# Performance work log

Hardware: AMD Instinct MI355X
Metric: run time of the kernel (lower is better)

The kernel has to match this reference:

```python
import jax, jax.numpy as jnp
import numpy as np

N = 1024
B = 128
DT = 0.1
STEPS = 10

def setup_inputs() -> dict:
    key = jax.random.key(0)
    k1, k2, k3 = jax.random.split(key, 3)
    theta_init = jax.random.normal(k1, (B, N), dtype=jnp.float32)
    K0 = jax.random.normal(k2, (N, N), dtype=jnp.float32) * 0.1
    K = (K0 + K0.T) / 2  # symmetric coupling matrix, as in __init__
    omega = jax.random.normal(k3, (N,), dtype=jnp.float32) * 0.1
    K_global = jnp.asarray(0.5, dtype=jnp.float32)
    return {"theta_init": theta_init, "K": K, "omega": omega, "K_global": K_global}

def _compute_coherence(theta):
    # Kuramoto order parameter r = |<e^{i theta}>| over oscillator axis
    cos_mean = jnp.cos(theta).mean(axis=-1)
    sin_mean = jnp.sin(theta).mean(axis=-1)
    return jnp.sqrt(cos_mean ** 2 + sin_mean ** 2)

def reference(theta_init, K, omega, K_global):
    n = theta_init.shape[-1]

    def step(theta, _):
        # theta_diff[b, i, j] = theta[b, j] - theta[b, i]
        theta_diff = theta[..., None, :] - theta[..., :, None]  # [B, n, n]
        coupling_sum = (K * jnp.sin(theta_diff)).sum(axis=-1)   # [B, n]
        dtheta = omega + (K_global / n) * coupling_sum
        theta_new = theta + DT * dtheta
        # wrap to (-pi, pi]
        theta_new = jnp.arctan2(jnp.sin(theta_new), jnp.cos(theta_new))
        return theta_new, None

    theta, _ = jax.lax.scan(step, theta_init, None, length=STEPS)
    coherence = _compute_coherence(theta)
    return theta, coherence
```

## Files before the change

### kernel.cpp

```cpp
#include <hip/hip_runtime.h>
#include <math.h>

#define KN 1024
#define KB 128
#define KDT 0.1f
#define KSTEPS 10
#define KMAGIC 0xB0000000u
#define PI_F 3.14159265358979f
#define TWO_PI_F 6.28318530717959f

typedef __attribute__((ext_vector_type(8))) short short8;
typedef __attribute__((ext_vector_type(4))) float floatx4;
typedef unsigned long long u64;

__device__ __forceinline__ unsigned short f2bf(float f) {
    unsigned u = __float_as_uint(f);
    u += 0x7FFF + ((u >> 16) & 1);
    return (unsigned short)(u >> 16);
}

__device__ __forceinline__ unsigned xidx(int grp, int b15, int k) {
    return (unsigned)(grp * 16384 + (k >> 5) * 512 + ((k >> 1) & 3) * 128 +
                      ((k >> 3) & 3) * 32 + b15 * 2 + (k & 1));
}

__global__ __launch_bounds__(512)
void k_main(const float* __restrict__ theta0,
            const float* __restrict__ Kmat,
            const float* __restrict__ omega,
            const float* __restrict__ kg,
            float* __restrict__ out_theta,
            float* __restrict__ out_coh,
            unsigned* __restrict__ flags,
            float* __restrict__ acc,
            unsigned* __restrict__ xA,
            unsigned* __restrict__ xB)
{
    const int grp = blockIdx.x >> 5;
    const int b0  = grp * 16;
    const int i0  = (blockIdx.x & 31) * 32;

    const int tid  = threadIdx.x;
    const int lane = tid & 63;
    const int kq   = tid >> 6;
    const int r16  = lane & 15;
    const int quad = lane >> 4;

    __shared__ float ldsY[8][2][16][34];

    if ((blockIdx.x & 31) == 0 && tid < 16) {
        __hip_atomic_store(&acc[(b0 + tid) * 16], 0.f, __ATOMIC_RELAXED,
                           __HIP_MEMORY_SCOPE_AGENT);
        __hip_atomic_store(&acc[2048 + (b0 + tid) * 16], 0.f, __ATOMIC_RELAXED,
                           __HIP_MEMORY_SCOPE_AGENT);
    }

    short8 bfrag[2][4];
    #pragma unroll
    for (int wi = 0; wi < 2; ++wi) {
        const float* kp = Kmat + (size_t)(i0 + wi * 16 + r16) * KN + kq * 128 + quad * 8;
        #pragma unroll
        for (int it = 0; it < 4; ++it) {
            const float4 v0 = *reinterpret_cast<const float4*>(kp + it * 32);
            const float4 v1 = *reinterpret_cast<const float4*>(kp + it * 32 + 4);
            short8 b_;
            b_[0] = (short)f2bf(v0.x); b_[1] = (short)f2bf(v0.y);
            b_[2] = (short)f2bf(v0.z); b_[3] = (short)f2bf(v0.w);
            b_[4] = (short)f2bf(v1.x); b_[5] = (short)f2bf(v1.y);
            b_[6] = (short)f2bf(v1.z); b_[7] = (short)f2bf(v1.w);
            bfrag[wi][it] = b_;
        }
    }

    const int eb = b0 + (tid >> 5);
    const int ei = i0 + (tid & 31);
    float th_reg = theta0[(size_t)eb * KN + ei];
    const float omg = omega[ei];
    float sn, cs;
    __sincosf(th_reg, &sn, &cs);
    __hip_atomic_store(&xA[xidx(grp, eb & 15, ei)],
                       (unsigned)f2bf(sn) | ((unsigned)f2bf(cs) << 16),
                       __ATOMIC_RELAXED, __HIP_MEMORY_SCOPE_AGENT);
    const float scale = kg[0] * (1.0f / (float)KN);

    __syncthreads();
    if (tid == 0)
        __hip_atomic_store(&flags[blockIdx.x], KMAGIC + 0u,
                           __ATOMIC_RELAXED, __HIP_MEMORY_SCOPE_AGENT);

    auto wait_chunks = [&](unsigned tgt) {
        unsigned polls = 0;
        for (;;) {
            unsigned v = tgt;
            if (lane < 4)
                v = __hip_atomic_load(&flags[grp * 32 + kq * 4 + lane],
                                      __ATOMIC_RELAXED, __HIP_MEMORY_SCOPE_AGENT);
            if (__ballot(v >= tgt) == ~0ull) break;
            if (++polls > 4000000u) break;
            __builtin_amdgcn_s_sleep(2);
        }
    };

    const unsigned* xcur = xA;
    unsigned* xnxt = xB;
    float s2 = sn, c2 = cs;
    for (int s = 0; s < KSTEPS; ++s) {
        wait_chunks(KMAGIC + (unsigned)s);

        const u64* xg = (const u64*)xcur + grp * 8192 + kq * 1024 + lane;
        u64 aw[4][4];
        #pragma unroll
        for (int it = 0; it < 4; ++it)
            #pragma unroll
            for (int jj = 0; jj < 4; ++jj)
                aw[it][jj] = __hip_atomic_load((u64*)(xg + it * 256 + jj * 64),
                                               __ATOMIC_RELAXED,
                                               __HIP_MEMORY_SCOPE_AGENT);
        floatx4 accS[2] = {{0.f,0.f,0.f,0.f},{0.f,0.f,0.f,0.f}};
        floatx4 accC[2] = {{0.f,0.f,0.f,0.f},{0.f,0.f,0.f,0.f}};
        #pragma unroll
        for (int it = 0; it < 4; ++it) {
            short8 a_s, a_c;
            #pragma unroll
            for (int jj = 0; jj < 4; ++jj) {
                unsigned lo = (unsigned)aw[it][jj];
                unsigned hi = (unsigned)(aw[it][jj] >> 32);
                a_s[jj * 2]     = (short)(lo & 0xffffu);
                a_c[jj * 2]     = (short)(lo >> 16);
                a_s[jj * 2 + 1] = (short)(hi & 0xffffu);
                a_c[jj * 2 + 1] = (short)(hi >> 16);
            }
            #pragma unroll
            for (int wi = 0; wi < 2; ++wi) {
                accS[wi] = __builtin_amdgcn_mfma_f32_16x16x32_bf16(a_s, bfrag[wi][it], accS[wi], 0, 0, 0);
                accC[wi] = __builtin_amdgcn_mfma_f32_16x16x32_bf16(a_c, bfrag[wi][it], accC[wi], 0, 0, 0);
            }
        }
        #pragma unroll
        for (int wi = 0; wi < 2; ++wi)
            #pragma unroll
            for (int r = 0; r < 4; ++r) {
                ldsY[kq][0][quad * 4 + r][wi * 16 + r16] = accS[wi][r];
                ldsY[kq][1][quad * 4 + r][wi * 16 + r16] = accC[wi][r];
            }
        __syncthreads();

        {
            const int bl = tid >> 5, ilo = tid & 31;
            float Ys = 0.f, Yc = 0.f;
            #pragma unroll
            for (int q = 0; q < 8; ++q) {
                Ys += ldsY[q][0][bl][ilo];
                Yc += ldsY[q][1][bl][ilo];
            }
            const float coupling = cs * Ys - sn * Yc;
            float tn = th_reg + KDT * (omg + scale * coupling);
            __sincosf(tn, &s2, &c2);
            if (tn > PI_F)       tn -= TWO_PI_F;
            else if (tn < -PI_F) tn += TWO_PI_F;
            th_reg = tn;
            sn = s2; cs = c2;
        }
        if (s < KSTEPS - 1) {
            __hip_atomic_store(&xnxt[xidx(grp, eb & 15, ei)],
                               (unsigned)f2bf(s2) | ((unsigned)f2bf(c2) << 16),
                               __ATOMIC_RELAXED, __HIP_MEMORY_SCOPE_AGENT);
            __syncthreads();
            if (tid == 0)
                __hip_atomic_store(&flags[blockIdx.x], KMAGIC + (unsigned)(s + 1),
                                   __ATOMIC_RELAXED, __HIP_MEMORY_SCOPE_AGENT);
            const unsigned* t = xcur; xcur = xnxt; xnxt = (unsigned*)t;
        } else {
            out_theta[(size_t)eb * KN + ei] = th_reg;
        }
    }

    __syncthreads();
    float* red = &ldsY[0][0][0][0];
    red[tid]       = s2;
    red[512 + tid] = c2;
    __syncthreads();
    if (tid < 16) {
        float ss = 0.f, cc = 0.f;
        #pragma unroll
        for (int il2 = 0; il2 < 32; ++il2) {
            ss += red[tid * 32 + il2];
            cc += red[512 + tid * 32 + il2];
        }
        atomicAdd(&acc[(b0 + tid) * 16], ss);
        atomicAdd(&acc[2048 + (b0 + tid) * 16], cc);
    }
    __syncthreads();
    if (tid == 0)
        __hip_atomic_store(&flags[blockIdx.x], KMAGIC + (unsigned)KSTEPS,
                           __ATOMIC_RELAXED, __HIP_MEMORY_SCOPE_AGENT);

    if ((blockIdx.x & 31) == 0) {
        if (tid < 64) {
            const unsigned tgt = KMAGIC + (unsigned)KSTEPS;
            unsigned polls = 0;
            for (;;) {
                unsigned v = tgt;
                if (lane < 32)
                    v = __hip_atomic_load(&flags[grp * 32 + lane],
                                          __ATOMIC_RELAXED, __HIP_MEMORY_SCOPE_AGENT);
                if (__ballot(v >= tgt) == ~0ull) break;
                if (++polls > 4000000u) break;
                __builtin_amdgcn_s_sleep(2);
            }
        }
        __syncthreads();
        if (tid < 16) {
            float sv = __hip_atomic_load(&acc[(b0 + tid) * 16],
                                         __ATOMIC_RELAXED, __HIP_MEMORY_SCOPE_AGENT);
            float cv = __hip_atomic_load(&acc[2048 + (b0 + tid) * 16],
                                         __ATOMIC_RELAXED, __HIP_MEMORY_SCOPE_AGENT);
            float sm = sv * (1.0f / (float)KN);
            float cm = cv * (1.0f / (float)KN);
            out_coh[b0 + tid] = sqrtf(cm * cm + sm * sm);
        }
    }
}

extern "C" void kernel_launch(void* const* d_in, const int* in_sizes, int n_in,
                              void* d_out, int out_size, void* d_ws, size_t ws_size,
                              hipStream_t stream)
{
    (void)in_sizes; (void)n_in; (void)out_size; (void)ws_size;

    const float* theta0 = (const float*)d_in[0];
    const float* Kmat   = (const float*)d_in[1];
    const float* omega  = (const float*)d_in[2];
    const float* kg     = (const float*)d_in[3];

    float* out_theta = (float*)d_out;
    float* out_coh   = out_theta + (size_t)KB * KN;

    unsigned* flags = (unsigned*)d_ws;
    float* acc      = (float*)((char*)d_ws + 4096);
    unsigned* xA    = (unsigned*)((char*)d_ws + 4096 + 16384);
    unsigned* xB    = xA + (size_t)KB * KN;

    k_main<<<256, 512, 0, stream>>>(theta0, Kmat, omega, kg,
                                    out_theta, out_coh, flags, acc, xA, xB);
}
```

Before: 97.89 us.

## Retile blocks to 8x64, use per-wave flags and multi-buffered exchange

Each block now covers 8 batch rows by 64 oscillators instead of 16 by 32. The packed sin/cos exchange buffer becomes separate bf16 sin and cos planes, so a single MFMA A operand carries sin rows and cos rows together. Readiness is tracked with one flag per wave instead of one per block, which drops the block-wide barrier before publishing, and the exchange buffer is rotated across up to 11 depths when workspace allows, avoiding write-after-read hazards between steps. This aims to cut the inter-block synchronisation latency per step, at the cost of polling more flags and relying on workspace size.

```diff
diff --git a/kernel.cpp b/kernel.cpp
--- a/kernel.cpp
+++ b/kernel.cpp
@@ -17,11 +17,6 @@
     unsigned u = __float_as_uint(f);
     u += 0x7FFF + ((u >> 16) & 1);
     return (unsigned short)(u >> 16);
-}
-
-__device__ __forceinline__ unsigned xidx(int grp, int b15, int k) {
-    return (unsigned)(grp * 16384 + (k >> 5) * 512 + ((k >> 1) & 3) * 128 +
-                      ((k >> 3) & 3) * 32 + b15 * 2 + (k & 1));
 }
 
 __global__ __launch_bounds__(512)
@@ -33,32 +28,34 @@
             float* __restrict__ out_coh,
             unsigned* __restrict__ flags,
             float* __restrict__ acc,
-            unsigned* __restrict__ xA,
-            unsigned* __restrict__ xB)
+            unsigned short* __restrict__ xbuf,
+            int depth)
 {
-    const int grp = blockIdx.x >> 5;
-    const int b0  = grp * 16;
-    const int i0  = (blockIdx.x & 31) * 32;
+    const int grp = blockIdx.x >> 4;
+    const int ib  = blockIdx.x & 15;
+    const int b0  = grp * 8;
+    const int i0  = ib * 64;
 
     const int tid  = threadIdx.x;
     const int lane = tid & 63;
-    const int kq   = tid >> 6;
+    const int wv   = tid >> 6;
     const int r16  = lane & 15;
     const int quad = lane >> 4;
-
-    __shared__ float ldsY[8][2][16][34];
-
-    if ((blockIdx.x & 31) == 0 && tid < 16) {
-        __hip_atomic_store(&acc[(b0 + tid) * 16], 0.f, __ATOMIC_RELAXED,
-                           __HIP_MEMORY_SCOPE_AGENT);
-        __hip_atomic_store(&acc[2048 + (b0 + tid) * 16], 0.f, __ATOMIC_RELAXED,
-                           __HIP_MEMORY_SCOPE_AGENT);
-    }
-
-    short8 bfrag[2][4];
+    const int ub  = lane >> 3;
+    const int ui  = i0 + wv * 8 + (lane & 7);
+    const int uil = wv * 8 + (lane & 7);
+
+    __shared__ float ldsY[8][16][68];
+
+    if (ib == 0 && tid < 8) {
+        __hip_atomic_store(&acc[(b0 + tid) * 16], 0.f, __ATOMIC_RELAXED, __HIP_MEMORY_SCOPE_AGENT);
+        __hip_atomic_store(&acc[2048 + (b0 + tid) * 16], 0.f, __ATOMIC_RELAXED, __HIP_MEMORY_SCOPE_AGENT);
+    }
+
+    short8 bfrag[4][4];
     #pragma unroll
-    for (int wi = 0; wi < 2; ++wi) {
-        const float* kp = Kmat + (size_t)(i0 + wi * 16 + r16) * KN + kq * 128 + quad * 8;
+    for (int sub = 0; sub < 4; ++sub) {
+        const float* kp = Kmat + (size_t)(i0 + sub * 16 + r16) * KN + wv * 128 + quad * 8;
         #pragma unroll
         for (int it = 0; it < 4; ++it) {
             const float4 v0 = *reinterpret_cast<const float4*>(kp + it * 32);
@@ -68,149 +65,129 @@
             b_[2] = (short)f2bf(v0.z); b_[3] = (short)f2bf(v0.w);
             b_[4] = (short)f2bf(v1.x); b_[5] = (short)f2bf(v1.y);
             b_[6] = (short)f2bf(v1.z); b_[7] = (short)f2bf(v1.w);
-            bfrag[wi][it] = b_;
-        }
-    }
-
-    const int eb = b0 + (tid >> 5);
-    const int ei = i0 + (tid & 31);
-    float th_reg = theta0[(size_t)eb * KN + ei];
-    const float omg = omega[ei];
+            bfrag[sub][it] = b_;
+        }
+    }
+
+    float th = theta0[(size_t)(b0 + ub) * KN + ui];
+    const float omg = omega[ui];
+    const float scale = kg[0] * (1.0f / (float)KN);
     float sn, cs;
-    __sincosf(th_reg, &sn, &cs);
-    __hip_atomic_store(&xA[xidx(grp, eb & 15, ei)],
-                       (unsigned)f2bf(sn) | ((unsigned)f2bf(cs) << 16),
-                       __ATOMIC_RELAXED, __HIP_MEMORY_SCOPE_AGENT);
-    const float scale = kg[0] * (1.0f / (float)KN);
-
-    __syncthreads();
-    if (tid == 0)
-        __hip_atomic_store(&flags[blockIdx.x], KMAGIC + 0u,
-                           __ATOMIC_RELAXED, __HIP_MEMORY_SCOPE_AGENT);
-
-    auto wait_chunks = [&](unsigned tgt) {
-        unsigned polls = 0;
-        for (;;) {
-            unsigned v = tgt;
-            if (lane < 4)
-                v = __hip_atomic_load(&flags[grp * 32 + kq * 4 + lane],
-                                      __ATOMIC_RELAXED, __HIP_MEMORY_SCOPE_AGENT);
-            if (__ballot(v >= tgt) == ~0ull) break;
-            if (++polls > 4000000u) break;
-            __builtin_amdgcn_s_sleep(2);
-        }
-    };
-
-    const unsigned* xcur = xA;
-    unsigned* xnxt = xB;
-    float s2 = sn, c2 = cs;
+    __sincosf(th, &sn, &cs);
+
+    const unsigned kblk = (unsigned)(ib * 8 + wv);
+    unsigned* myflag = &flags[grp * 128 + ib * 8 + wv];
+
+    {
+        unsigned short* xp = xbuf + (size_t)grp * 16384 + (size_t)kblk * 128;
+        __hip_atomic_store(&xp[lane],      f2bf(sn), __ATOMIC_RELAXED, __HIP_MEMORY_SCOPE_AGENT);
+        __hip_atomic_store(&xp[64 + lane], f2bf(cs), __ATOMIC_RELAXED, __HIP_MEMORY_SCOPE_AGENT);
+        __builtin_amdgcn_s_waitcnt(0x0F70);
+        if (lane == 0)
+            __hip_atomic_store(myflag, KMAGIC + 0u, __ATOMIC_RELAXED, __HIP_MEMORY_SCOPE_AGENT);
+    }
+
+    floatx4 accv[4];
     for (int s = 0; s < KSTEPS; ++s) {
-        wait_chunks(KMAGIC + (unsigned)s);
-
-        const u64* xg = (const u64*)xcur + grp * 8192 + kq * 1024 + lane;
-        u64 aw[4][4];
-        #pragma unroll
-        for (int it = 0; it < 4; ++it)
+        {
+            const unsigned tgt = KMAGIC + (unsigned)s;
+            unsigned polls = 0;
+            for (;;) {
+                unsigned v = tgt;
+                if (lane < 16)
+                    v = __hip_atomic_load(&flags[grp * 128 + wv * 16 + lane],
+                                          __ATOMIC_RELAXED, __HIP_MEMORY_SCOPE_AGENT);
+                if (__ballot(v >= tgt) == ~0ull) break;
+                if (++polls > 8000000u) break;
+                __builtin_amdgcn_s_sleep(1);
+            }
+        }
+        const u64* xg = (const u64*)(xbuf + (size_t)(s % depth) * 262144) + grp * 4096 + r16 * 2;
+        u64 aw[4][2];
+        #pragma unroll
+        for (int it = 0; it < 4; ++it) {
+            const u64* p = xg + (size_t)(wv * 16 + it * 4 + quad) * 32;
+            aw[it][0] = __hip_atomic_load((u64*)p,       __ATOMIC_RELAXED, __HIP_MEMORY_SCOPE_AGENT);
+            aw[it][1] = __hip_atomic_load((u64*)(p + 1), __ATOMIC_RELAXED, __HIP_MEMORY_SCOPE_AGENT);
+        }
+        #pragma unroll
+        for (int sub = 0; sub < 4; ++sub) accv[sub] = (floatx4){0.f, 0.f, 0.f, 0.f};
+        #pragma unroll
+        for (int it = 0; it < 4; ++it) {
+            union { u64 q[2]; short8 s8; } ua;
+            ua.q[0] = aw[it][0]; ua.q[1] = aw[it][1];
             #pragma unroll
-            for (int jj = 0; jj < 4; ++jj)
-                aw[it][jj] = __hip_atomic_load((u64*)(xg + it * 256 + jj * 64),
-                                               __ATOMIC_RELAXED,
-                                               __HIP_MEMORY_SCOPE_AGENT);
-        floatx4 accS[2] = {{0.f,0.f,0.f,0.f},{0.f,0.f,0.f,0.f}};
-        floatx4 accC[2] = {{0.f,0.f,0.f,0.f},{0.f,0.f,0.f,0.f}};
-        #pragma unroll
-        for (int it = 0; it < 4; ++it) {
-            short8 a_s, a_c;
+            for (int sub = 0; sub < 4; ++sub)
+                accv[sub] = __builtin_amdgcn_mfma_f32_16x16x32_bf16(ua.s8, bfrag[sub][it], accv[sub], 0, 0, 0);
+        }
+        #pragma unroll
+        for (int sub = 0; sub < 4; ++sub)
             #pragma unroll
-            for (int jj = 0; jj < 4; ++jj) {
-                unsigned lo = (unsigned)aw[it][jj];
-                unsigned hi = (unsigned)(aw[it][jj] >> 32);
-                a_s[jj * 2]     = (short)(lo & 0xffffu);
-                a_c[jj * 2]     = (short)(lo >> 16);
-                a_s[jj * 2 + 1] = (short)(hi & 0xffffu);
-                a_c[jj * 2 + 1] = (short)(hi >> 16);
-            }
-            #pragma unroll
-            for (int wi = 0; wi < 2; ++wi) {
-                accS[wi] = __builtin_amdgcn_mfma_f32_16x16x32_bf16(a_s, bfrag[wi][it], accS[wi], 0, 0, 0);
-                accC[wi] = __builtin_amdgcn_mfma_f32_16x16x32_bf16(a_c, bfrag[wi][it], accC[wi], 0, 0, 0);
-            }
-        }
-        #pragma unroll
-        for (int wi = 0; wi < 2; ++wi)
-            #pragma unroll
-            for (int r = 0; r < 4; ++r) {
-                ldsY[kq][0][quad * 4 + r][wi * 16 + r16] = accS[wi][r];
-                ldsY[kq][1][quad * 4 + r][wi * 16 + r16] = accC[wi][r];
-            }
+            for (int r = 0; r < 4; ++r)
+                ldsY[wv][quad * 4 + r][sub * 16 + r16] = accv[sub][r];
         __syncthreads();
 
         {
-            const int bl = tid >> 5, ilo = tid & 31;
             float Ys = 0.f, Yc = 0.f;
             #pragma unroll
             for (int q = 0; q < 8; ++q) {
-                Ys += ldsY[q][0][bl][ilo];
-                Yc += ldsY[q][1][bl][ilo];
+                Ys += ldsY[q][ub][uil];
+                Yc += ldsY[q][8 + ub][uil];
             }
             const float coupling = cs * Ys - sn * Yc;
-            float tn = th_reg + KDT * (omg + scale * coupling);
+            float tn = th + KDT * (omg + scale * coupling);
+            float s2, c2;
             __sincosf(tn, &s2, &c2);
             if (tn > PI_F)       tn -= TWO_PI_F;
             else if (tn < -PI_F) tn += TWO_PI_F;
-            th_reg = tn;
-            sn = s2; cs = c2;
+            th = tn; sn = s2; cs = c2;
         }
         if (s < KSTEPS - 1) {
-            __hip_atomic_store(&xnxt[xidx(grp, eb & 15, ei)],
-                               (unsigned)f2bf(s2) | ((unsigned)f2bf(c2) << 16),
-                               __ATOMIC_RELAXED, __HIP_MEMORY_SCOPE_AGENT);
-            __syncthreads();
-            if (tid == 0)
-                __hip_atomic_store(&flags[blockIdx.x], KMAGIC + (unsigned)(s + 1),
+            unsigned short* xp = xbuf + (size_t)((s + 1) % depth) * 262144
+                               + (size_t)grp * 16384 + (size_t)kblk * 128;
+            __hip_atomic_store(&xp[lane],      f2bf(sn), __ATOMIC_RELAXED, __HIP_MEMORY_SCOPE_AGENT);
+            __hip_atomic_store(&xp[64 + lane], f2bf(cs), __ATOMIC_RELAXED, __HIP_MEMORY_SCOPE_AGENT);
+            __builtin_amdgcn_s_waitcnt(0x0F70);
+            if (lane == 0)
+                __hip_atomic_store(myflag, KMAGIC + (unsigned)(s + 1),
                                    __ATOMIC_RELAXED, __HIP_MEMORY_SCOPE_AGENT);
-            const unsigned* t = xcur; xcur = xnxt; xnxt = (unsigned*)t;
-        } else {
-            out_theta[(size_t)eb * KN + ei] = th_reg;
-        }
-    }
-
+        }
+        __syncthreads();
+    }
+
+    out_theta[(size_t)(b0 + ub) * KN + ui] = th;
+
+    ldsY[0][ub][uil] = sn;
+    ldsY[1][ub][uil] = cs;
     __syncthreads();
-    float* red = &ldsY[0][0][0][0];
-    red[tid]       = s2;
-    red[512 + tid] = c2;
-    __syncthreads();
-    if (tid < 16) {
+    if (tid < 8) {
         float ss = 0.f, cc = 0.f;
-        #pragma unroll
-        for (int il2 = 0; il2 < 32; ++il2) {
-            ss += red[tid * 32 + il2];
-            cc += red[512 + tid * 32 + il2];
-        }
+        for (int c = 0; c < 64; ++c) { ss += ldsY[0][tid][c]; cc += ldsY[1][tid][c]; }
         atomicAdd(&acc[(b0 + tid) * 16], ss);
         atomicAdd(&acc[2048 + (b0 + tid) * 16], cc);
     }
+    __builtin_amdgcn_s_waitcnt(0x0F70);
     __syncthreads();
-    if (tid == 0)
-        __hip_atomic_store(&flags[blockIdx.x], KMAGIC + (unsigned)KSTEPS,
+    if (lane == 0)
+        __hip_atomic_store(myflag, KMAGIC + (unsigned)KSTEPS,
                            __ATOMIC_RELAXED, __HIP_MEMORY_SCOPE_AGENT);
 
-    if ((blockIdx.x & 31) == 0) {
-        if (tid < 64) {
+    if (ib == 0) {
+        if (wv == 0) {
             const unsigned tgt = KMAGIC + (unsigned)KSTEPS;
             unsigned polls = 0;
             for (;;) {
-                unsigned v = tgt;
-                if (lane < 32)
-                    v = __hip_atomic_load(&flags[grp * 32 + lane],
-                                          __ATOMIC_RELAXED, __HIP_MEMORY_SCOPE_AGENT);
-                if (__ballot(v >= tgt) == ~0ull) break;
-                if (++polls > 4000000u) break;
-                __builtin_amdgcn_s_sleep(2);
+                unsigned v0 = __hip_atomic_load(&flags[grp * 128 + lane],
+                                                __ATOMIC_RELAXED, __HIP_MEMORY_SCOPE_AGENT);
+                unsigned v1 = __hip_atomic_load(&flags[grp * 128 + 64 + lane],
+                                                __ATOMIC_RELAXED, __HIP_MEMORY_SCOPE_AGENT);
+                if (__ballot(v0 >= tgt && v1 >= tgt) == ~0ull) break;
+                if (++polls > 8000000u) break;
+                __builtin_amdgcn_s_sleep(1);
             }
         }
         __syncthreads();
-        if (tid < 16) {
+        if (tid < 8) {
             float sv = __hip_atomic_load(&acc[(b0 + tid) * 16],
                                          __ATOMIC_RELAXED, __HIP_MEMORY_SCOPE_AGENT);
             float cv = __hip_atomic_load(&acc[2048 + (b0 + tid) * 16],
@@ -226,7 +203,7 @@
                               void* d_out, int out_size, void* d_ws, size_t ws_size,
                               hipStream_t stream)
 {
-    (void)in_sizes; (void)n_in; (void)out_size; (void)ws_size;
+    (void)in_sizes; (void)n_in; (void)out_size;
 
     const float* theta0 = (const float*)d_in[0];
     const float* Kmat   = (const float*)d_in[1];
@@ -236,11 +213,15 @@
     float* out_theta = (float*)d_out;
     float* out_coh   = out_theta + (size_t)KB * KN;
 
-    unsigned* flags = (unsigned*)d_ws;
-    float* acc      = (float*)((char*)d_ws + 4096);
-    unsigned* xA    = (unsigned*)((char*)d_ws + 4096 + 16384);
-    unsigned* xB    = xA + (size_t)KB * KN;
+    unsigned* flags      = (unsigned*)d_ws;
+    float* acc           = (float*)((char*)d_ws + 8192);
+    unsigned short* xbuf = (unsigned short*)((char*)d_ws + 24576);
+
+    const size_t base = 24576;
+    int depth = 2;
+    if (ws_size >= base + 11u * 524288u)      depth = 11;
+    else if (ws_size >= base + 3u * 524288u)  depth = 3;
 
     k_main<<<256, 512, 0, stream>>>(theta0, Kmat, omega, kg,
-                                    out_theta, out_coh, flags, acc, xA, xB);
+                                    out_theta, out_coh, flags, acc, xbuf, depth);
 }
```

Measured after the change: 104.1 us. 1.06x slower.
